# Optimization experiments

Hardware: AMD Instinct MI355X
Metric: run time of the kernel (lower is better)

## Reference

```python
import jax, jax.numpy as jnp
import numpy as np

LEAKY_SLOPE = 0.2
N_HEADS = 8
INPUT_DIM = 128
HEAD_DIM = 16  # embed_dim=128 // n_heads=8


def setup_inputs() -> dict:
    key = jax.random.key(0)
    k1, k2, k3, k4 = jax.random.split(key, 4)
    b, n = 4, 512
    h = jax.random.normal(k1, (b, n, INPUT_DIM), dtype=jnp.float32)
    mask = jnp.zeros((b, n, n), dtype=bool)  # 1 = attention not possible
    stdv_w = 1.0 / np.sqrt(HEAD_DIM)
    Wl = jax.random.uniform(k2, (N_HEADS, INPUT_DIM, HEAD_DIM), minval=-stdv_w, maxval=stdv_w, dtype=jnp.float32)
    Wr = jax.random.uniform(k3, (N_HEADS, INPUT_DIM, HEAD_DIM), minval=-stdv_w, maxval=stdv_w, dtype=jnp.float32)
    # Wak in torch is (n_heads, head_dim, 1); stdv = 1/sqrt(size(-1)) = 1
    Wak = jax.random.uniform(k4, (N_HEADS, HEAD_DIM), minval=-1.0, maxval=1.0, dtype=jnp.float32)
    return {"h": h, "mask": mask, "Wl": Wl, "Wr": Wr, "Wak": Wak}


def reference(h, mask, Wl, Wr, Wak):
    b, n, _ = h.shape
    # per-head projections: g = h @ W  -> (heads, batch, N, head_dim)
    g_l = jnp.einsum('bni,hid->hbnd', h, Wl)
    g_r = jnp.einsum('bni,hid->hbnd', h, Wr)
    # additive attention: LeakyReLU(g_l_i + g_r_j) . a  -> (heads, batch, N, N)
    e = jax.nn.leaky_relu(g_l[:, :, :, None, :] + g_r[:, :, None, :, :],
                          negative_slope=LEAKY_SLOPE)
    scores = jnp.einsum('hbijd,hd->hbij', e, Wak)
    scores = jnp.where(mask[None], -jnp.inf, scores)
    attn = jax.nn.softmax(scores, axis=-1)
    # weighted sum of g_r, then ReLU; output layout (batch, N, heads*head_dim)
    h_prime = jax.nn.relu(jnp.einsum('hbij,hbjd->bihd', attn, g_r))
    return h_prime.reshape(b, n, -1)
```

## Files before the change

kernel.cpp:

```cpp
#include <hip/hip_runtime.h>
#include <hip/hip_bf16.h>

#define B_SZ 4
#define N_SZ 512
#define IN_DIM 128
#define NH 8
#define HD 16
#define SLOPE 0.2f

#define ROWS 32
#define JT   16
#define TPB  512
#define GR_STRIDE 20
#define GLS_STRIDE 20

typedef float v2f __attribute__((ext_vector_type(2)));

#define WS_GL 0
#define WS_GR (NH * B_SZ * N_SZ * HD)
#define WS_TOT (2 * WS_GR)

#define PM 32
#define PKC 64
#define AT_S 38
#define BT_S 68

__global__ __launch_bounds__(256) void proj_gemm(
    const float* __restrict__ hin, const float* __restrict__ Wl,
    const float* __restrict__ Wr, float* __restrict__ gl, float* __restrict__ gr)
{
    __shared__ float At[PKC * AT_S];
    __shared__ float Bs[PKC * BT_S];

    int rt = blockIdx.x >> 2;
    int ct = blockIdx.x & 3;
    int side = ct >> 1;
    int headbase = (ct & 1) * 4;
    const float* Wsrc = side ? Wr : Wl;
    int rowbase = rt * PM;

    int t = threadIdx.x;
    int ty = t >> 4;
    int tx = t & 15;

    float acc[2][4] = {{0.f,0.f,0.f,0.f},{0.f,0.f,0.f,0.f}};

    for (int kc = 0; kc < IN_DIM; kc += PKC) {
        __syncthreads();
#pragma unroll
        for (int it = 0; it < 2; ++it) {
            int task = it * 256 + t;
            int r = task >> 4, kq = task & 15;
            float4 v = *(const float4*)&hin[(size_t)(rowbase + r) * IN_DIM + kc + kq * 4];
            At[(kq * 4 + 0) * AT_S + r] = v.x;
            At[(kq * 4 + 1) * AT_S + r] = v.y;
            At[(kq * 4 + 2) * AT_S + r] = v.z;
            At[(kq * 4 + 3) * AT_S + r] = v.w;
        }
#pragma unroll
        for (int it = 0; it < 4; ++it) {
            int task = it * 256 + t;
            int k = task >> 4, cc4 = task & 15;
            int head = headbase + (cc4 >> 2);
            int dq = (cc4 & 3) * 4;
            float4 v = *(const float4*)&Wsrc[head * (IN_DIM * HD) + (kc + k) * HD + dq];
            *(float4*)&Bs[k * BT_S + cc4 * 4] = v;
        }
        __syncthreads();

#pragma unroll 16
        for (int k = 0; k < PKC; ++k) {
            float2 a = *(const float2*)&At[k * AT_S + ty * 2];
            float4 b = *(const float4*)&Bs[k * BT_S + tx * 4];
            acc[0][0] = fmaf(a.x, b.x, acc[0][0]);
            acc[0][1] = fmaf(a.x, b.y, acc[0][1]);
            acc[0][2] = fmaf(a.x, b.z, acc[0][2]);
            acc[0][3] = fmaf(a.x, b.w, acc[0][3]);
            acc[1][0] = fmaf(a.y, b.x, acc[1][0]);
            acc[1][1] = fmaf(a.y, b.y, acc[1][1]);
            acc[1][2] = fmaf(a.y, b.z, acc[1][2]);
            acc[1][3] = fmaf(a.y, b.w, acc[1][3]);
        }
    }

    int head = headbase + (tx >> 2);
    int d4 = (tx & 3) * 4;
    float* g = side ? gr : gl;
#pragma unroll
    for (int r = 0; r < 2; ++r) {
        int row = rowbase + ty * 2 + r;
        int b = row >> 9, i = row & (N_SZ - 1);
        float4 v = {acc[r][0], acc[r][1], acc[r][2], acc[r][3]};
        *(float4*)&g[((size_t)(head * B_SZ + b) * N_SZ + i) * HD + d4] = v;
    }
}

__global__ __launch_bounds__(TPB, 4) void attn_kernel(
    const float* __restrict__ gl, const float* __restrict__ gr,
    const float* __restrict__ Wak, const unsigned char* __restrict__ mask,
    float* __restrict__ out)
{
    __shared__ float grs[N_SZ * GR_STRIDE];
    __shared__ float gls[ROWS * GLS_STRIDE];
    __shared__ float crs[N_SZ];

    int bid = blockIdx.x;
    int itile = bid & 15;
    int hb = bid >> 4;
    int head = hb >> 2, b = hb & 3;
    int t = threadIdx.x;

    int il = t >> 4;
    int jt = t & 15;
    int i = itile * ROWS + il;

    const float* grp = gr + (size_t)hb * (N_SZ * HD);
#pragma unroll
    for (int it = 0; it < 4; ++it) {
        int idx4 = it * TPB + t;
        float4 v = ((const float4*)grp)[idx4];
        int j = idx4 >> 2, dq = (idx4 & 3) * 4;
        *(float4*)&grs[j * GR_STRIDE + dq] = v;
    }
    const float* glp = gl + ((size_t)hb * N_SZ + itile * ROWS) * HD;
    {
        int row = t >> 4, d = t & 15;
        gls[row * GLS_STRIDE + d] = glp[t];
    }

    const unsigned char* mrow = mask + ((size_t)(b * N_SZ + i)) * N_SZ;
    unsigned mbits = 0;
#pragma unroll
    for (int jj = 0; jj < N_SZ / JT; ++jj)
        mbits |= (mrow[jj * JT + jt] ? 1u : 0u) << jj;

    __syncthreads();

    const float* ap = Wak + head * HD;

    {
        const float* r = &grs[t * GR_STRIDE];
        float acc = 0.f;
#pragma unroll
        for (int dd = 0; dd < HD; ++dd) acc = fmaf(ap[dd], r[dd], acc);
        crs[t] = 0.6f * acc;
    }

    v2f glv[HD / 2], o[HD / 2];
    const float* grow = &gls[il * GLS_STRIDE];
#pragma unroll
    for (int e = 0; e < HD / 2; ++e) glv[e] = *(const v2f*)(grow + 2 * e);
    float cl06;
    {
        float acc = 0.f;
#pragma unroll
        for (int dd = 0; dd < HD; ++dd) acc = fmaf(ap[dd], grow[dd], acc);
        cl06 = 0.6f * acc;
    }
#pragma unroll
    for (int e = 0; e < HD / 2; ++e) o[e] = (v2f){0.f, 0.f};

    __syncthreads();

    float l = 0.f;

#pragma unroll 2
    for (int jj = 0; jj < N_SZ / JT; ++jj) {
        int j = jj * JT + jt;
        const float* r = &grs[j * GR_STRIDE];
        float4 g01 = *(const float4*)(r);
        float4 g23 = *(const float4*)(r + 4);
        float4 g45 = *(const float4*)(r + 8);
        float4 g67 = *(const float4*)(r + 12);
        v2f gj[HD / 2] = {
            (v2f){g01.x, g01.y}, (v2f){g01.z, g01.w},
            (v2f){g23.x, g23.y}, (v2f){g23.z, g23.w},
            (v2f){g45.x, g45.y}, (v2f){g45.z, g45.w},
            (v2f){g67.x, g67.y}, (v2f){g67.z, g67.w}};

        float s0 = 0.f, s1 = 0.f;
#pragma unroll
        for (int e = 0; e < HD / 2; ++e) {
            v2f x = glv[e] + gj[e];
            s0 = fmaf(ap[2 * e],     fabsf(x.x), s0);
            s1 = fmaf(ap[2 * e + 1], fabsf(x.y), s1);
        }
        float s = fmaf(0.4f, s0 + s1, cl06 + crs[j]);
        s = fminf(s, 80.f);
        if (mbits & (1u << jj)) s = -1e30f;

        float p = __expf(s);
        l += p;
        v2f pv = (v2f){p, p};
#pragma unroll
        for (int e = 0; e < HD / 2; ++e)
            o[e] += pv * gj[e];
    }

#pragma unroll
    for (int off = 1; off < JT; off <<= 1) {
        l += __shfl_xor(l, off, 64);
#pragma unroll
        for (int e = 0; e < HD / 2; ++e) {
            v2f other;
            other.x = __shfl_xor(o[e].x, off, 64);
            other.y = __shfl_xor(o[e].y, off, 64);
            o[e] += other;
        }
    }

    if (jt == 0) {
        float inv = 1.f / l;
        float res[HD];
#pragma unroll
        for (int e = 0; e < HD / 2; ++e) {
            res[2 * e]     = fmaxf(o[e].x * inv, 0.f);
            res[2 * e + 1] = fmaxf(o[e].y * inv, 0.f);
        }
        float* op = out + ((size_t)(b * N_SZ + i)) * (NH * HD) + head * HD;
        *(float4*)op = *(float4*)res;
        *(float4*)(op + 4) = *(float4*)(res + 4);
        *(float4*)(op + 8) = *(float4*)(res + 8);
        *(float4*)(op + 12) = *(float4*)(res + 12);
    }
}

__global__ __launch_bounds__(TPB) void gatv2_fused(
    const float* __restrict__ hin, const unsigned char* __restrict__ mask,
    const float* __restrict__ Wl, const float* __restrict__ Wr,
    const float* __restrict__ Wak, float* __restrict__ out)
{
    __shared__ float wrs[IN_DIM * HD];
    __shared__ float hsh[32][IN_DIM + 1];
    __shared__ float grs[N_SZ * 18];
    __shared__ float gls[32][HD];

    int bid = blockIdx.x;
    int itile = bid & 15;
    int hb = bid >> 4;
    int head = hb >> 2, b = hb & 3;
    int t = threadIdx.x;

    int jl = t >> 4;
    int d  = t & 15;

    for (int idx = t; idx < IN_DIM * HD; idx += TPB)
        wrs[idx] = Wr[head * IN_DIM * HD + idx];

    const float* hb_base = hin + (size_t)b * N_SZ * IN_DIM;
    const float* wlcol = Wl + head * IN_DIM * HD + d;

    for (int c = 0; c < N_SZ / 32; ++c) {
        __syncthreads();
        const float* hc = hb_base + (size_t)c * 32 * IN_DIM;
        for (int idx = t; idx < 32 * IN_DIM; idx += TPB)
            hsh[idx >> 7][idx & 127] = hc[idx];
        __syncthreads();

        float acc = 0.f;
#pragma unroll 16
        for (int k = 0; k < IN_DIM; ++k)
            acc = fmaf(hsh[jl][k], wrs[k * HD + d], acc);
        grs[(c * 32 + jl) * 18 + d] = acc;

        if (c == itile) {
            float accl = 0.f;
#pragma unroll 16
            for (int k = 0; k < IN_DIM; ++k)
                accl = fmaf(hsh[jl][k], wlcol[k * HD], accl);
            gls[jl][d] = accl;
        }
    }
    __syncthreads();

    int il = jl, jt = d;
    int i = itile * 32 + il;

    float glv[HD], avv[HD];
#pragma unroll
    for (int dd = 0; dd < HD; ++dd) glv[dd] = gls[il][dd];
    const float* ap = Wak + head * HD;
#pragma unroll
    for (int dd = 0; dd < HD; ++dd) avv[dd] = ap[dd];

    const unsigned char* mrow = mask + ((size_t)(b * N_SZ + i)) * N_SZ;

    float m = -1e30f, l = 0.f;
    float o[HD];
#pragma unroll
    for (int dd = 0; dd < HD; ++dd) o[dd] = 0.f;

    for (int jj = 0; jj < N_SZ / 16; ++jj) {
        int j = jj * 16 + jt;
        const float* r = &grs[j * 18];
        float gj[HD];
#pragma unroll
        for (int e = 0; e < HD / 2; ++e) {
            float2 v = *(const float2*)(r + 2 * e);
            gj[2 * e] = v.x; gj[2 * e + 1] = v.y;
        }

        float s = 0.f;
#pragma unroll
        for (int dd = 0; dd < HD; ++dd) {
            float x = glv[dd] + gj[dd];
            float lr = fmaxf(x, SLOPE * x);
            s = fmaf(avv[dd], lr, s);
        }
        if (mrow[j]) s = -1e30f;

        float mn = fmaxf(m, s);
        float cc = __expf(m - mn);
        float p = __expf(s - mn);
        l = fmaf(l, cc, p);
#pragma unroll
        for (int dd = 0; dd < HD; ++dd)
            o[dd] = fmaf(o[dd], cc, p * gj[dd]);
        m = mn;
    }

#pragma unroll
    for (int off = 1; off < 16; off <<= 1) {
        float mo = __shfl_xor(m, off, 64);
        float lo = __shfl_xor(l, off, 64);
        float mn = fmaxf(m, mo);
        float c1 = __expf(m - mn), c2 = __expf(mo - mn);
        l = l * c1 + lo * c2;
#pragma unroll
        for (int dd = 0; dd < HD; ++dd)
            o[dd] = o[dd] * c1 + __shfl_xor(o[dd], off, 64) * c2;
        m = mn;
    }

    if (jt == 0) {
        float inv = 1.f / l;
        float res[HD];
#pragma unroll
        for (int dd = 0; dd < HD; ++dd)
            res[dd] = fmaxf(o[dd] * inv, 0.f);
        float* op = out + ((size_t)(b * N_SZ + i)) * (NH * HD) + head * HD;
#pragma unroll
        for (int e = 0; e < HD / 4; ++e)
            *(float4*)(op + 4 * e) = *(float4*)(res + 4 * e);
    }
}

extern "C" void kernel_launch(void* const* d_in, const int* in_sizes, int n_in,
                              void* d_out, int out_size, void* d_ws, size_t ws_size,
                              hipStream_t stream) {
    const float* hin = (const float*)d_in[0];
    const unsigned char* mask = (const unsigned char*)d_in[1];
    const float* Wl = (const float*)d_in[2];
    const float* Wr = (const float*)d_in[3];
    const float* Wak = (const float*)d_in[4];
    float* out = (float*)d_out;
    (void)in_sizes; (void)n_in; (void)out_size;

    const size_t need = (size_t)WS_TOT * sizeof(float);

    if (ws_size >= need && d_ws != nullptr) {
        float* ws = (float*)d_ws;
        float* gl = ws + WS_GL;
        float* gr = ws + WS_GR;
        proj_gemm<<<(B_SZ * N_SZ / PM) * 4, 256, 0, stream>>>(hin, Wl, Wr, gl, gr);
        attn_kernel<<<NH * B_SZ * (N_SZ / ROWS), TPB, 0, stream>>>(
            gl, gr, Wak, mask, out);
    } else {
        gatv2_fused<<<NH * B_SZ * (N_SZ / 32), TPB, 0, stream>>>(
            hin, mask, Wl, Wr, Wak, out);
    }
}
```

Baseline: 86.52 us.

## Process two query rows per thread to reuse gr loads, reduce partials via LDS

Each thread now handles two query rows i against 32-way strided key columns, so each gr row fetched from shared memory is reused for two score and accumulate computations. This halves the LDS traffic per unit of arithmetic. The cross-lane reduction is cut to two shuffle steps, and the remaining eight partial sums per row are combined through shared memory, reusing the grs buffer. In exchange, register pressure roughly doubles for the accumulators, which may hurt occupancy under the 4-blocks launch bound, and two extra barriers are added.

```diff
diff --git a/kernel.cpp b/kernel.cpp
--- a/kernel.cpp
+++ b/kernel.cpp
@@ -9,7 +9,6 @@
 #define SLOPE 0.2f
 
 #define ROWS 32
-#define JT   16
 #define TPB  512
 #define GR_STRIDE 20
 #define GLS_STRIDE 20
@@ -110,9 +109,9 @@
     int head = hb >> 2, b = hb & 3;
     int t = threadIdx.x;
 
-    int il = t >> 4;
-    int jt = t & 15;
-    int i = itile * ROWS + il;
+    int ig = t >> 5;
+    int jt = t & 31;
+    int i0 = itile * ROWS + ig * 2;
 
     const float* grp = gr + (size_t)hb * (N_SZ * HD);
 #pragma unroll
@@ -123,16 +122,15 @@
         *(float4*)&grs[j * GR_STRIDE + dq] = v;
     }
     const float* glp = gl + ((size_t)hb * N_SZ + itile * ROWS) * HD;
-    {
-        int row = t >> 4, d = t & 15;
-        gls[row * GLS_STRIDE + d] = glp[t];
-    }
-
-    const unsigned char* mrow = mask + ((size_t)(b * N_SZ + i)) * N_SZ;
-    unsigned mbits = 0;
-#pragma unroll
-    for (int jj = 0; jj < N_SZ / JT; ++jj)
-        mbits |= (mrow[jj * JT + jt] ? 1u : 0u) << jj;
+    gls[(t >> 4) * GLS_STRIDE + (t & 15)] = glp[t];
+
+    const unsigned char* mrow0 = mask + ((size_t)(b * N_SZ + i0)) * N_SZ;
+    unsigned mb0 = 0, mb1 = 0;
+#pragma unroll
+    for (int jj = 0; jj < N_SZ / 32; ++jj) {
+        mb0 |= (mrow0[jj * 32 + jt] ? 1u : 0u) << jj;
+        mb1 |= (mrow0[N_SZ + jj * 32 + jt] ? 1u : 0u) << jj;
+    }
 
     __syncthreads();
 
@@ -146,27 +144,34 @@
         crs[t] = 0.6f * acc;
     }
 
-    v2f glv[HD / 2], o[HD / 2];
-    const float* grow = &gls[il * GLS_STRIDE];
-#pragma unroll
-    for (int e = 0; e < HD / 2; ++e) glv[e] = *(const v2f*)(grow + 2 * e);
-    float cl06;
+    v2f glv0[HD / 2], glv1[HD / 2], o0[HD / 2], o1[HD / 2];
+    const float* grow0 = &gls[(ig * 2) * GLS_STRIDE];
+    const float* grow1 = grow0 + GLS_STRIDE;
+#pragma unroll
+    for (int e = 0; e < HD / 2; ++e) {
+        glv0[e] = *(const v2f*)(grow0 + 2 * e);
+        glv1[e] = *(const v2f*)(grow1 + 2 * e);
+        o0[e] = (v2f){0.f, 0.f};
+        o1[e] = (v2f){0.f, 0.f};
+    }
+    float cl0, cl1;
     {
-        float acc = 0.f;
-#pragma unroll
-        for (int dd = 0; dd < HD; ++dd) acc = fmaf(ap[dd], grow[dd], acc);
-        cl06 = 0.6f * acc;
-    }
-#pragma unroll
-    for (int e = 0; e < HD / 2; ++e) o[e] = (v2f){0.f, 0.f};
+        float a0 = 0.f, a1 = 0.f;
+#pragma unroll
+        for (int dd = 0; dd < HD; ++dd) {
+            a0 = fmaf(ap[dd], grow0[dd], a0);
+            a1 = fmaf(ap[dd], grow1[dd], a1);
+        }
+        cl0 = 0.6f * a0; cl1 = 0.6f * a1;
+    }
 
     __syncthreads();
 
-    float l = 0.f;
+    float l0 = 0.f, l1 = 0.f;
 
 #pragma unroll 2
-    for (int jj = 0; jj < N_SZ / JT; ++jj) {
-        int j = jj * JT + jt;
+    for (int jj = 0; jj < N_SZ / 32; ++jj) {
+        int j = jj * 32 + jt;
         const float* r = &grs[j * GR_STRIDE];
         float4 g01 = *(const float4*)(r);
         float4 g23 = *(const float4*)(r + 4);
@@ -177,51 +182,85 @@
             (v2f){g23.x, g23.y}, (v2f){g23.z, g23.w},
             (v2f){g45.x, g45.y}, (v2f){g45.z, g45.w},
             (v2f){g67.x, g67.y}, (v2f){g67.z, g67.w}};
-
-        float s0 = 0.f, s1 = 0.f;
+        float crj = crs[j];
+
+        float s0a = 0.f, s0b = 0.f, s1a = 0.f, s1b = 0.f;
 #pragma unroll
         for (int e = 0; e < HD / 2; ++e) {
-            v2f x = glv[e] + gj[e];
-            s0 = fmaf(ap[2 * e],     fabsf(x.x), s0);
-            s1 = fmaf(ap[2 * e + 1], fabsf(x.y), s1);
-        }
-        float s = fmaf(0.4f, s0 + s1, cl06 + crs[j]);
-        s = fminf(s, 80.f);
-        if (mbits & (1u << jj)) s = -1e30f;
-
-        float p = __expf(s);
-        l += p;
-        v2f pv = (v2f){p, p};
-#pragma unroll
-        for (int e = 0; e < HD / 2; ++e)
-            o[e] += pv * gj[e];
-    }
-
-#pragma unroll
-    for (int off = 1; off < JT; off <<= 1) {
-        l += __shfl_xor(l, off, 64);
+            v2f x0 = glv0[e] + gj[e];
+            v2f x1 = glv1[e] + gj[e];
+            s0a = fmaf(ap[2 * e],     fabsf(x0.x), s0a);
+            s0b = fmaf(ap[2 * e + 1], fabsf(x0.y), s0b);
+            s1a = fmaf(ap[2 * e],     fabsf(x1.x), s1a);
+            s1b = fmaf(ap[2 * e + 1], fabsf(x1.y), s1b);
+        }
+        float s0 = fminf(fmaf(0.4f, s0a + s0b, cl0 + crj), 80.f);
+        float s1 = fminf(fmaf(0.4f, s1a + s1b, cl1 + crj), 80.f);
+        if (mb0 & (1u << jj)) s0 = -1e30f;
+        if (mb1 & (1u << jj)) s1 = -1e30f;
+
+        float p0 = __expf(s0);
+        float p1 = __expf(s1);
+        l0 += p0; l1 += p1;
+        v2f pv0 = (v2f){p0, p0}, pv1 = (v2f){p1, p1};
 #pragma unroll
         for (int e = 0; e < HD / 2; ++e) {
-            v2f other;
-            other.x = __shfl_xor(o[e].x, off, 64);
-            other.y = __shfl_xor(o[e].y, off, 64);
-            o[e] += other;
-        }
-    }
-
-    if (jt == 0) {
-        float inv = 1.f / l;
-        float res[HD];
+            o0[e] += pv0 * gj[e];
+            o1[e] += pv1 * gj[e];
+        }
+    }
+
+#pragma unroll
+    for (int off = 1; off < 4; off <<= 1) {
+        l0 += __shfl_xor(l0, off, 64);
+        l1 += __shfl_xor(l1, off, 64);
 #pragma unroll
         for (int e = 0; e < HD / 2; ++e) {
-            res[2 * e]     = fmaxf(o[e].x * inv, 0.f);
-            res[2 * e + 1] = fmaxf(o[e].y * inv, 0.f);
-        }
-        float* op = out + ((size_t)(b * N_SZ + i)) * (NH * HD) + head * HD;
-        *(float4*)op = *(float4*)res;
-        *(float4*)(op + 4) = *(float4*)(res + 4);
-        *(float4*)(op + 8) = *(float4*)(res + 8);
-        *(float4*)(op + 12) = *(float4*)(res + 12);
+            v2f q0, q1;
+            q0.x = __shfl_xor(o0[e].x, off, 64);
+            q0.y = __shfl_xor(o0[e].y, off, 64);
+            q1.x = __shfl_xor(o1[e].x, off, 64);
+            q1.y = __shfl_xor(o1[e].y, off, 64);
+            o0[e] += q0;
+            o1[e] += q1;
+        }
+    }
+
+    __syncthreads();
+
+    float* po = grs;
+    float* pl = grs + 32 * 8 * GR_STRIDE;
+    if ((jt & 3) == 0) {
+        int g = jt >> 2;
+        int r0 = (ig * 2) * 8 + g;
+        int r1 = r0 + 8;
+        float res0[HD], res1[HD];
+#pragma unroll
+        for (int e = 0; e < HD / 2; ++e) {
+            res0[2 * e] = o0[e].x; res0[2 * e + 1] = o0[e].y;
+            res1[2 * e] = o1[e].x; res1[2 * e + 1] = o1[e].y;
+        }
+#pragma unroll
+        for (int q = 0; q < 4; ++q) {
+            *(float4*)&po[r0 * GR_STRIDE + 4 * q] = *(float4*)&res0[4 * q];
+            *(float4*)&po[r1 * GR_STRIDE + 4 * q] = *(float4*)&res1[4 * q];
+        }
+        pl[r0] = l0;
+        pl[r1] = l1;
+    }
+    __syncthreads();
+
+    {
+        int il = t >> 4, d = t & 15;
+        float os = 0.f, ls = 0.f;
+#pragma unroll
+        for (int g = 0; g < 8; ++g) {
+            os += po[(il * 8 + g) * GR_STRIDE + d];
+            ls += pl[il * 8 + g];
+        }
+        int i = itile * ROWS + il;
+        out[((size_t)(b * N_SZ + i)) * (NH * HD) + head * HD + d] =
+            fmaxf(os / ls, 0.f);
     }
 }
 
```

Measured after the change: 87.32 us. About the same (+0.9%).

## Replace shared-memory attention kernel with wave-per-row-pair register kernel

Applied to the files above, without the earlier changes.

The attention kernel is rewritten so each 64-lane wave handles two query rows. Lanes split the head dimension in halves and partial scores are combined with shuffles. Key vectors are streamed directly from global memory instead of staged in LDS, which removes the shared-memory fill, barriers and per-block setup, and increases the block count. The trade-off is more global/L2 traffic, since every wave rereads all of gr, plus per-iteration shuffles and byte mask loads.

```diff
diff --git a/kernel.cpp b/kernel.cpp
--- a/kernel.cpp
+++ b/kernel.cpp
@@ -7,12 +7,6 @@
 #define NH 8
 #define HD 16
 #define SLOPE 0.2f
-
-#define ROWS 32
-#define JT   16
-#define TPB  512
-#define GR_STRIDE 20
-#define GLS_STRIDE 20
 
 typedef float v2f __attribute__((ext_vector_type(2)));
 
@@ -95,137 +89,115 @@
     }
 }
 
-__global__ __launch_bounds__(TPB, 4) void attn_kernel(
+__global__ __launch_bounds__(256) void attn_wave(
     const float* __restrict__ gl, const float* __restrict__ gr,
     const float* __restrict__ Wak, const unsigned char* __restrict__ mask,
     float* __restrict__ out)
 {
-    __shared__ float grs[N_SZ * GR_STRIDE];
-    __shared__ float gls[ROWS * GLS_STRIDE];
-    __shared__ float crs[N_SZ];
-
     int bid = blockIdx.x;
-    int itile = bid & 15;
-    int hb = bid >> 4;
+    int hb = bid >> 6;
     int head = hb >> 2, b = hb & 3;
     int t = threadIdx.x;
-
-    int il = t >> 4;
-    int jt = t & 15;
-    int i = itile * ROWS + il;
-
-    const float* grp = gr + (size_t)hb * (N_SZ * HD);
-#pragma unroll
-    for (int it = 0; it < 4; ++it) {
-        int idx4 = it * TPB + t;
-        float4 v = ((const float4*)grp)[idx4];
-        int j = idx4 >> 2, dq = (idx4 & 3) * 4;
-        *(float4*)&grs[j * GR_STRIDE + dq] = v;
-    }
-    const float* glp = gl + ((size_t)hb * N_SZ + itile * ROWS) * HD;
+    int wv = t >> 6;
+    int lane = t & 63;
+    int jh = lane >> 1;
+    int h = lane & 1;
+
+    int pair = (bid & 63) * 4 + wv;
+    int i0 = pair * 2;
+
+    const float* grb = gr + (size_t)hb * (N_SZ * HD);
+    const float* gl0 = gl + ((size_t)hb * N_SZ + i0) * HD;
+    const float* ap = Wak + head * HD;
+
+    float a[8], w0[8], w1[8];
     {
-        int row = t >> 4, d = t & 15;
-        gls[row * GLS_STRIDE + d] = glp[t];
-    }
-
-    const unsigned char* mrow = mask + ((size_t)(b * N_SZ + i)) * N_SZ;
-    unsigned mbits = 0;
-#pragma unroll
-    for (int jj = 0; jj < N_SZ / JT; ++jj)
-        mbits |= (mrow[jj * JT + jt] ? 1u : 0u) << jj;
-
-    __syncthreads();
-
-    const float* ap = Wak + head * HD;
-
-    {
-        const float* r = &grs[t * GR_STRIDE];
-        float acc = 0.f;
-#pragma unroll
-        for (int dd = 0; dd < HD; ++dd) acc = fmaf(ap[dd], r[dd], acc);
-        crs[t] = 0.6f * acc;
-    }
-
-    v2f glv[HD / 2], o[HD / 2];
-    const float* grow = &gls[il * GLS_STRIDE];
-#pragma unroll
-    for (int e = 0; e < HD / 2; ++e) glv[e] = *(const v2f*)(grow + 2 * e);
-    float cl06;
-    {
-        float acc = 0.f;
-#pragma unroll
-        for (int dd = 0; dd < HD; ++dd) acc = fmaf(ap[dd], grow[dd], acc);
-        cl06 = 0.6f * acc;
-    }
-#pragma unroll
-    for (int e = 0; e < HD / 2; ++e) o[e] = (v2f){0.f, 0.f};
-
-    __syncthreads();
-
-    float l = 0.f;
-
-#pragma unroll 2
-    for (int jj = 0; jj < N_SZ / JT; ++jj) {
-        int j = jj * JT + jt;
-        const float* r = &grs[j * GR_STRIDE];
-        float4 g01 = *(const float4*)(r);
-        float4 g23 = *(const float4*)(r + 4);
-        float4 g45 = *(const float4*)(r + 8);
-        float4 g67 = *(const float4*)(r + 12);
-        v2f gj[HD / 2] = {
-            (v2f){g01.x, g01.y}, (v2f){g01.z, g01.w},
-            (v2f){g23.x, g23.y}, (v2f){g23.z, g23.w},
-            (v2f){g45.x, g45.y}, (v2f){g45.z, g45.w},
-            (v2f){g67.x, g67.y}, (v2f){g67.z, g67.w}};
-
-        float s0 = 0.f, s1 = 0.f;
-#pragma unroll
-        for (int e = 0; e < HD / 2; ++e) {
-            v2f x = glv[e] + gj[e];
-            s0 = fmaf(ap[2 * e],     fabsf(x.x), s0);
-            s1 = fmaf(ap[2 * e + 1], fabsf(x.y), s1);
-        }
-        float s = fmaf(0.4f, s0 + s1, cl06 + crs[j]);
-        s = fminf(s, 80.f);
-        if (mbits & (1u << jj)) s = -1e30f;
-
-        float p = __expf(s);
-        l += p;
-        v2f pv = (v2f){p, p};
-#pragma unroll
-        for (int e = 0; e < HD / 2; ++e)
-            o[e] += pv * gj[e];
-    }
-
-#pragma unroll
-    for (int off = 1; off < JT; off <<= 1) {
-        l += __shfl_xor(l, off, 64);
-#pragma unroll
-        for (int e = 0; e < HD / 2; ++e) {
-            v2f other;
-            other.x = __shfl_xor(o[e].x, off, 64);
-            other.y = __shfl_xor(o[e].y, off, 64);
-            o[e] += other;
-        }
-    }
-
-    if (jt == 0) {
-        float inv = 1.f / l;
-        float res[HD];
-#pragma unroll
-        for (int e = 0; e < HD / 2; ++e) {
-            res[2 * e]     = fmaxf(o[e].x * inv, 0.f);
-            res[2 * e + 1] = fmaxf(o[e].y * inv, 0.f);
-        }
-        float* op = out + ((size_t)(b * N_SZ + i)) * (NH * HD) + head * HD;
+        float4 a0 = *(const float4*)(ap + h * 8);
+        float4 a1 = *(const float4*)(ap + h * 8 + 4);
+        float4 u0 = *(const float4*)(gl0 + h * 8);
+        float4 u1 = *(const float4*)(gl0 + h * 8 + 4);
+        float4 v0 = *(const float4*)(gl0 + HD + h * 8);
+        float4 v1 = *(const float4*)(gl0 + HD + h * 8 + 4);
+        a[0]=a0.x; a[1]=a0.y; a[2]=a0.z; a[3]=a0.w;
+        a[4]=a1.x; a[5]=a1.y; a[6]=a1.z; a[7]=a1.w;
+        w0[0]=u0.x; w0[1]=u0.y; w0[2]=u0.z; w0[3]=u0.w;
+        w0[4]=u1.x; w0[5]=u1.y; w0[6]=u1.z; w0[7]=u1.w;
+        w1[0]=v0.x; w1[1]=v0.y; w1[2]=v0.z; w1[3]=v0.w;
+        w1[4]=v1.x; w1[5]=v1.y; w1[6]=v1.z; w1[7]=v1.w;
+    }
+
+    const unsigned char* m0p = mask + ((size_t)(b * N_SZ + i0)) * N_SZ;
+    const unsigned char* m1p = m0p + N_SZ;
+
+    float o0[8], o1[8];
+#pragma unroll
+    for (int k = 0; k < 8; ++k) { o0[k] = 0.f; o1[k] = 0.f; }
+    float l0 = 0.f, l1 = 0.f;
+
+#pragma unroll 4
+    for (int it = 0; it < N_SZ / 32; ++it) {
+        int j = it * 32 + jh;
+        const float* src = grb + it * 512 + lane * 8;
+        float4 ga = *(const float4*)src;
+        float4 gb = *(const float4*)(src + 4);
+        float g[8] = {ga.x, ga.y, ga.z, ga.w, gb.x, gb.y, gb.z, gb.w};
+
+        float u = 0.f, s0p = 0.f, s1p = 0.f;
+#pragma unroll
+        for (int k = 0; k < 8; ++k) {
+            u = fmaf(a[k], g[k], u);
+            s0p = fmaf(a[k], fabsf(w0[k] + g[k]), s0p);
+            s1p = fmaf(a[k], fabsf(w1[k] + g[k]), s1p);
+        }
+        float u06 = 0.6f * u;
+        float s0 = fmaf(0.4f, s0p, u06);
+        float s1 = fmaf(0.4f, s1p, u06);
+        s0 += __shfl_xor(s0, 1, 64);
+        s1 += __shfl_xor(s1, 1, 64);
+
+        unsigned char mm0 = m0p[j];
+        unsigned char mm1 = m1p[j];
+        s0 = mm0 ? -1e30f : fminf(s0, 80.f);
+        s1 = mm1 ? -1e30f : fminf(s1, 80.f);
+
+        float p0 = __expf(s0);
+        float p1 = __expf(s1);
+        l0 += p0; l1 += p1;
+#pragma unroll
+        for (int k = 0; k < 8; ++k) {
+            o0[k] = fmaf(p0, g[k], o0[k]);
+            o1[k] = fmaf(p1, g[k], o1[k]);
+        }
+    }
+
+#pragma unroll
+    for (int off = 2; off < 64; off <<= 1) {
+        l0 += __shfl_xor(l0, off, 64);
+        l1 += __shfl_xor(l1, off, 64);
+#pragma unroll
+        for (int k = 0; k < 8; ++k) {
+            o0[k] += __shfl_xor(o0[k], off, 64);
+            o1[k] += __shfl_xor(o1[k], off, 64);
+        }
+    }
+
+    if (lane < 4) {
+        int r = lane >> 1;
+        float li = r ? l1 : l0;
+        float inv = 1.f / li;
+        const float* oo = r ? o1 : o0;
+        float res[8];
+#pragma unroll
+        for (int k = 0; k < 8; ++k)
+            res[k] = fmaxf(oo[k] * inv, 0.f);
+        float* op = out + ((size_t)(b * N_SZ + i0 + r)) * (NH * HD)
+                        + head * HD + (lane & 1) * 8;
         *(float4*)op = *(float4*)res;
         *(float4*)(op + 4) = *(float4*)(res + 4);
-        *(float4*)(op + 8) = *(float4*)(res + 8);
-        *(float4*)(op + 12) = *(float4*)(res + 12);
     }
 }
 
-__global__ __launch_bounds__(TPB) void gatv2_fused(
+__global__ __launch_bounds__(512) void gatv2_fused(
     const float* __restrict__ hin, const unsigned char* __restrict__ mask,
     const float* __restrict__ Wl, const float* __restrict__ Wr,
     const float* __restrict__ Wak, float* __restrict__ out)
@@ -244,7 +216,7 @@
     int jl = t >> 4;
     int d  = t & 15;
 
-    for (int idx = t; idx < IN_DIM * HD; idx += TPB)
+    for (int idx = t; idx < IN_DIM * HD; idx += 512)
         wrs[idx] = Wr[head * IN_DIM * HD + idx];
 
     const float* hb_base = hin + (size_t)b * N_SZ * IN_DIM;
@@ -253,7 +225,7 @@
     for (int c = 0; c < N_SZ / 32; ++c) {
         __syncthreads();
         const float* hc = hb_base + (size_t)c * 32 * IN_DIM;
-        for (int idx = t; idx < 32 * IN_DIM; idx += TPB)
+        for (int idx = t; idx < 32 * IN_DIM; idx += 512)
             hsh[idx >> 7][idx & 127] = hc[idx];
         __syncthreads();
 
@@ -363,10 +335,9 @@
         float* gl = ws + WS_GL;
         float* gr = ws + WS_GR;
         proj_gemm<<<(B_SZ * N_SZ / PM) * 4, 256, 0, stream>>>(hin, Wl, Wr, gl, gr);
-        attn_kernel<<<NH * B_SZ * (N_SZ / ROWS), TPB, 0, stream>>>(
-            gl, gr, Wak, mask, out);
+        attn_wave<<<NH * B_SZ * 64, 256, 0, stream>>>(gl, gr, Wak, mask, out);
     } else {
-        gatv2_fused<<<NH * B_SZ * (N_SZ / 32), TPB, 0, stream>>>(
+        gatv2_fused<<<NH * B_SZ * (N_SZ / 32), 512, 0, stream>>>(
             hin, mask, Wl, Wr, Wak, out);
     }
 }
```

New measurement: 89.64 us. 1.04x slower.
